# Kernel tuning notes

Measured on AMD Instinct MI355X. Metric: run time of the kernel, lower is better.

## Reference

```python
import jax, jax.numpy as jnp
import numpy as np

C = 1.5          # Poincare ball curvature (geoopt PoincareBallExact(c=1.5))
TEMP = 0.1       # logits temperature
EPS = 1e-5       # artanh clamp, matches geoopt fp32 eps


def _mlp(x, w1, b1, w2, b2, w3, b3):
    # torch nn.GELU default is the exact erf formulation
    h = jax.nn.gelu(x @ w1 + b1, approximate=False)
    h = jax.nn.gelu(h @ w2 + b2, approximate=False)
    return h @ w3 + b3


def _expmap0(u):
    # geoopt expmap0: tanh(sqrt(c)*||u||) * u / (sqrt(c)*||u||)
    sqrt_c = jnp.sqrt(C)
    n = jnp.maximum(jnp.linalg.norm(u, axis=-1, keepdims=True), 1e-15)
    return jnp.tanh(sqrt_c * n) * u / (sqrt_c * n)


def _poincare_dist(protos, y):
    """Pairwise Poincare distance. protos: (P, d) on-ball, y: (B, d) on-ball -> (B, P).
    dist(x, y) = 2/sqrt(c) * artanh(sqrt(c) * ||mobius_add(-x, y)||)
    """
    sqrt_c = jnp.sqrt(C)
    x = -protos                               # (P, d)
    x2 = jnp.sum(x * x, axis=-1)              # (P,)
    y2 = jnp.sum(y * y, axis=-1)              # (B,)
    xy = y @ x.T                              # (B, P) = <x, y> broadcast
    a = 1.0 + 2.0 * C * xy + C * y2[:, None]  # coeff of x
    b = 1.0 - C * x2[None, :]                 # coeff of y
    denom = 1.0 + 2.0 * C * xy + (C * C) * x2[None, :] * y2[:, None]
    denom = jnp.maximum(jnp.abs(denom), 1e-15)
    # only one (B, P, d) intermediate: the mobius-add numerator
    num = a[:, :, None] * x[None, :, :] + b[:, :, None] * y[:, None, :]
    r = sqrt_c * jnp.linalg.norm(num, axis=-1) / denom   # (B, P)
    r = jnp.clip(r, 0.0, 1.0 - EPS)
    return (2.0 / sqrt_c) * jnp.arctanh(r)


def setup_inputs() -> dict:
    key = jax.random.key(0)
    ks = jax.random.split(key, 16)
    B, DIN, H, D = 64, 768, 4096, 256
    PG, PS = 500, 5000

    def lin(kw, kb, fan_in, fan_out):
        s = 1.0 / np.sqrt(fan_in)
        w = jax.random.uniform(kw, (fan_in, fan_out), jnp.float32, -s, s)
        b = jax.random.uniform(kb, (fan_out,), jnp.float32, -s, s)
        return w, b

    x = jax.random.normal(ks[0], (B, DIN), jnp.float32)
    # prototypes: random points well inside the ball (radius 1/sqrt(1.5) ~ 0.816)
    protos_genus = 0.01 * jax.random.normal(ks[1], (PG, D), jnp.float32)
    protos_species = 0.01 * jax.random.normal(ks[2], (PS, D), jnp.float32)

    w1g, b1g = lin(ks[3], ks[4], DIN, H)
    w2g, b2g = lin(ks[5], ks[6], H, H)
    w3g, b3g = lin(ks[7], ks[8], H, D)
    w1s, b1s = lin(ks[9], ks[10], DIN, H)
    w2s, b2s = lin(ks[11], ks[12], H, H)
    w3s, b3s = lin(ks[13], ks[14], H, D)

    return {
        "x": x, "protos_genus": protos_genus, "protos_species": protos_species,
        "w1g": w1g, "b1g": b1g, "w2g": w2g, "b2g": b2g, "w3g": w3g, "b3g": b3g,
        "w1s": w1s, "b1s": b1s, "w2s": w2s, "b2s": b2s, "w3s": w3s, "b3s": b3s,
    }


def reference(x, protos_genus, protos_species,
              w1g, b1g, w2g, b2g, w3g, b3g,
              w1s, b1s, w2s, b2s, w3s, b3s):
    feat_g = _mlp(x, w1g, b1g, w2g, b2g, w3g, b3g)   # (B, D) euclidean
    feat_s = _mlp(x, w1s, b1s, w2s, b2s, w3s, b3s)
    hyp_g = _expmap0(feat_g)
    hyp_s = _expmap0(feat_s)
    logits_g = -_poincare_dist(protos_genus, hyp_g) / TEMP    # (B, PG)
    logits_s = -_poincare_dist(protos_species, hyp_s) / TEMP  # (B, PS)
    return (logits_g, logits_s)
```

## Files before the change

kernel.cpp:

```cpp
#include <hip/hip_runtime.h>
#include <hip/hip_bf16.h>
#include <math.h>

typedef unsigned short ushort_t;
typedef unsigned int uint_t;

#define C_CURV 1.5f
#define SQRT_C 1.22474487139158905f
#define TEMP_ 0.1f

typedef __attribute__((ext_vector_type(8))) short short8;
typedef __attribute__((ext_vector_type(4))) float f32x4;

static __device__ __forceinline__ ushort_t f2bf(float f) {
  union { float f; uint_t u; } v; v.f = f;
  uint_t u = v.u;
  uint_t r = (u + 0x7FFFu + ((u >> 16) & 1u)) >> 16;
  return (ushort_t)r;
}

static __device__ __forceinline__ float b2f(ushort_t h) {
  union { uint_t u; float f; } v; v.u = ((uint_t)h) << 16;
  return v.f;
}

static __device__ __forceinline__ float gelu_exact(float x) {
  return 0.5f * x * (1.0f + erff(x * 0.70710678118654752f));
}

__global__ void k_cvt_x(const float* __restrict__ x, ushort_t* __restrict__ xb, int n4) {
  int i = blockIdx.x * blockDim.x + threadIdx.x;
  if (i >= n4) return;
  float4 v = reinterpret_cast<const float4*>(x)[i];
  ushort4 o;
  o.x = f2bf(v.x); o.y = f2bf(v.y); o.z = f2bf(v.z); o.w = f2bf(v.w);
  reinterpret_cast<ushort4*>(xb)[i] = o;
}

__global__ __launch_bounds__(512, 4) void k_gemm(
    const ushort_t* __restrict__ Abase, long a_br_stride,
    const float* __restrict__ Wg, const float* __restrict__ Ws,
    ushort_t* __restrict__ partial, int N, int K, int kchunk)
{
  __shared__ float    sW[2][64][128];
  __shared__ ushort_t sA[2][64][64];

  const int tn = blockIdx.x, ks = blockIdx.y, br = blockIdx.z;
  const int KS = gridDim.y;
  const ushort_t* A = Abase + (long)br * a_br_stride;
  const float* W = br ? Ws : Wg;
  const int tid = threadIdx.x;
  const int lane = tid & 63;
  const int w = tid >> 6;
  const int c = lane & 15;
  const int g = lane >> 4;
  const int n0b = tn * 128;
  const int k0 = ks * kchunk;

  const int srow = tid >> 3;
  const int wcol = (tid & 7) * 16;
  const int akoff = (tid & 7) * 8;

  const float* wst = W + (long)(k0 + srow) * N + n0b + wcol;
  const ushort_t* ast = A + (long)srow * K + k0 + akoff;

  f32x4 acc[4];
  #pragma unroll
  for (int mi = 0; mi < 4; ++mi) acc[mi] = f32x4{0.f, 0.f, 0.f, 0.f};

  float4 wvA0, wvA1, wvA2, wvA3; uint4 avA;
  float4 wvB0, wvB1, wvB2, wvB3; uint4 avB;
  float4 wvC0, wvC1, wvC2, wvC3; uint4 avC;

#define LOADREG(S, T) do { \
    const float* wp_ = wst + (long)((T) * 64) * N; \
    wv##S##0 = *reinterpret_cast<const float4*>(wp_); \
    wv##S##1 = *reinterpret_cast<const float4*>(wp_ + 4); \
    wv##S##2 = *reinterpret_cast<const float4*>(wp_ + 8); \
    wv##S##3 = *reinterpret_cast<const float4*>(wp_ + 12); \
    av##S = *reinterpret_cast<const uint4*>(ast + (T) * 64); \
  } while (0)

#define DSWRITE(S, B) do { \
    float4* wd_ = reinterpret_cast<float4*>(&sW[B][srow][wcol]); \
    wd_[0] = wv##S##0; wd_[1] = wv##S##1; wd_[2] = wv##S##2; wd_[3] = wv##S##3; \
    *reinterpret_cast<uint4*>(&sA[B][srow][akoff]) = av##S; \
  } while (0)

#define COMPUTE(B) do { \
    _Pragma("unroll") for (int kk = 0; kk < 64; kk += 32) { \
      short8 af[4]; \
      _Pragma("unroll") for (int mi = 0; mi < 4; ++mi) \
        af[mi] = *reinterpret_cast<const short8*>(&sA[B][c + 16 * mi][kk + 8 * g]); \
      float bw[8]; \
      _Pragma("unroll") for (int j = 0; j < 8; ++j) \
        bw[j] = sW[B][kk + 8 * g + j][w * 16 + c]; \
      short8 bf; \
      _Pragma("unroll") for (int j = 0; j < 8; ++j) bf[j] = (short)f2bf(bw[j]); \
      _Pragma("unroll") for (int mi = 0; mi < 4; ++mi) \
        acc[mi] = __builtin_amdgcn_mfma_f32_16x16x32_bf16(af[mi], bf, acc[mi], 0, 0, 0); \
    } \
  } while (0)

#define ITER(CUR, NXT2, T) do { \
    if ((T) + 2 < nt) LOADREG(NXT2, (T) + 2); \
    __builtin_amdgcn_sched_barrier(0); \
    DSWRITE(CUR, (T) & 1); \
    asm volatile("s_waitcnt lgkmcnt(0)" ::: "memory"); \
    __builtin_amdgcn_sched_barrier(0); \
    __builtin_amdgcn_s_barrier(); \
    __builtin_amdgcn_sched_barrier(0); \
    COMPUTE((T) & 1); \
  } while (0)

  const int nt = kchunk >> 6;
  LOADREG(A, 0);
  if (nt > 1) LOADREG(B, 1);
  for (int t = 0; t < nt; t += 3) {
    ITER(A, C, t);
    if (t + 1 < nt) ITER(B, A, t + 1);
    if (t + 2 < nt) ITER(C, B, t + 2);
  }
#undef LOADREG
#undef DSWRITE
#undef COMPUTE
#undef ITER

  ushort_t* po = partial + (long)(br * KS + ks) * 64 * N;
  const int n0 = n0b + w * 16 + c;
  #pragma unroll
  for (int mi = 0; mi < 4; ++mi)
    #pragma unroll
    for (int q = 0; q < 4; ++q) {
      int b = 16 * mi + 4 * g + q;
      po[(long)b * N + n0] = f2bf(acc[mi][q]);
    }
}

__global__ void k_reduce_gelu(const ushort_t* __restrict__ partial,
    const float* __restrict__ bg, const float* __restrict__ bs,
    ushort_t* __restrict__ hb, int N, int KS, int total8)
{
  int i = blockIdx.x * blockDim.x + threadIdx.x;
  if (i >= total8) return;
  int perbr8 = 64 * N / 8;
  int br = i / perbr8;
  int rem = i - br * perbr8;
  const short8* pp = reinterpret_cast<const short8*>(partial) + (long)br * KS * perbr8 + rem;
  float s[8] = {0.f, 0.f, 0.f, 0.f, 0.f, 0.f, 0.f, 0.f};
  for (int ks = 0; ks < KS; ++ks) {
    short8 t = pp[(long)ks * perbr8];
    #pragma unroll
    for (int j = 0; j < 8; ++j) s[j] += b2f((ushort_t)t[j]);
  }
  int n8 = rem % (N / 8);
  float4 bv0 = reinterpret_cast<const float4*>(br ? bs : bg)[n8 * 2];
  float4 bv1 = reinterpret_cast<const float4*>(br ? bs : bg)[n8 * 2 + 1];
  s[0] += bv0.x; s[1] += bv0.y; s[2] += bv0.z; s[3] += bv0.w;
  s[4] += bv1.x; s[5] += bv1.y; s[6] += bv1.z; s[7] += bv1.w;
  short8 o;
  #pragma unroll
  for (int j = 0; j < 8; ++j) o[j] = (short)f2bf(gelu_exact(s[j]));
  reinterpret_cast<short8*>(hb)[i] = o;
}

__global__ __launch_bounds__(256) void k_expmap(const ushort_t* __restrict__ partial,
    const float* __restrict__ b3g, const float* __restrict__ b3s,
    ushort_t* __restrict__ hypb, float* __restrict__ y2, int KS)
{
  int b = blockIdx.x, br = blockIdx.y, d = threadIdx.x;
  const ushort_t* pp = partial + (long)(br * KS) * 64 * 256 + (long)b * 256 + d;
  float s = 0.f;
  #pragma unroll 8
  for (int ks = 0; ks < KS; ++ks) s += b2f(pp[(long)ks * 64 * 256]);
  s += (br ? b3s : b3g)[d];

  float v = s * s;
  #pragma unroll
  for (int off = 1; off < 64; off <<= 1) v += __shfl_xor(v, off);
  __shared__ float red[4];
  __shared__ float n2s;
  if ((threadIdx.x & 63) == 0) red[threadIdx.x >> 6] = v;
  __syncthreads();
  if (threadIdx.x == 0) n2s = red[0] + red[1] + red[2] + red[3];
  __syncthreads();
  float n = fmaxf(sqrtf(n2s), 1e-15f);
  float sn = SQRT_C * n;
  float t = tanhf(sn);
  float scale = t / sn;
  hypb[((long)br * 64 + b) * 256 + d] = f2bf(s * scale);
  if (threadIdx.x == 0) y2[br * 64 + b] = t * t / C_CURV;
}

__global__ __launch_bounds__(256) void k_dist(const float* __restrict__ pg,
    const float* __restrict__ ps, const ushort_t* __restrict__ hypb,
    const float* __restrict__ y2, float* __restrict__ out)
{
  int u = blockIdx.x * 4 + (threadIdx.x >> 6);
  const int lane = threadIdx.x & 63;
  const int c = lane & 15, g = lane >> 4;
  const float* protos; const ushort_t* A; const float* y2p; float* ob; int P;
  if (u < 128) {
    protos = pg; P = 500; A = hypb; y2p = y2; ob = out;
  } else {
    u -= 128;
    if (u >= 1252) return;
    protos = ps; P = 5000; A = hypb + 64 * 256; y2p = y2 + 64; ob = out + 64 * 500;
  }
  const int w = u >> 2;
  const int mi = u & 3;
  int p = w * 16 + c;
  int pc = min(p, P - 1);
  const float* pp = protos + (long)pc * 256 + 8 * g;
  const ushort_t* ap = A + (long)(c + 16 * mi) * 256 + 8 * g;

  f32x4 acc = {0.f, 0.f, 0.f, 0.f};
  float x2p = 0.f;

  #pragma unroll
  for (int s8 = 0; s8 < 8; ++s8) {
    float4 v0 = *reinterpret_cast<const float4*>(pp + 32 * s8);
    float4 v1 = *reinterpret_cast<const float4*>(pp + 32 * s8 + 4);
    x2p += v0.x * v0.x + v0.y * v0.y + v0.z * v0.z + v0.w * v0.w
         + v1.x * v1.x + v1.y * v1.y + v1.z * v1.z + v1.w * v1.w;
    short8 bfr;
    bfr[0] = (short)f2bf(v0.x); bfr[1] = (short)f2bf(v0.y);
    bfr[2] = (short)f2bf(v0.z); bfr[3] = (short)f2bf(v0.w);
    bfr[4] = (short)f2bf(v1.x); bfr[5] = (short)f2bf(v1.y);
    bfr[6] = (short)f2bf(v1.z); bfr[7] = (short)f2bf(v1.w);
    short8 af = *reinterpret_cast<const short8*>(ap + 32 * s8);
    acc = __builtin_amdgcn_mfma_f32_16x16x32_bf16(af, bfr, acc, 0, 0, 0);
  }
  x2p += __shfl_xor(x2p, 16);
  x2p += __shfl_xor(x2p, 32);
  const float x2 = x2p;
  const float bb = 1.f - C_CURV * x2;
  const float LC = -2.f / (SQRT_C * TEMP_);

  if (p < P) {
    #pragma unroll
    for (int q = 0; q < 4; ++q) {
      int b = 16 * mi + 4 * g + q;
      float xy = -acc[q];
      float y2v = y2p[b];
      float a = 1.f + 2.f * C_CURV * xy + C_CURV * y2v;
      float den = fabsf(1.f + 2.f * C_CURV * xy + C_CURV * C_CURV * x2 * y2v);
      den = fmaxf(den, 1e-15f);
      float num2 = a * a * x2 + 2.f * a * bb * xy + bb * bb * y2v;
      num2 = fmaxf(num2, 0.f);
      float r = SQRT_C * sqrtf(num2) / den;
      r = fminf(r, 1.f - 1e-5f);
      r = fmaxf(r, 0.f);
      ob[(long)b * P + p] = LC * atanhf(r);
    }
  }
}

extern "C" void kernel_launch(void* const* d_in, const int* in_sizes, int n_in,
                              void* d_out, int out_size, void* d_ws, size_t ws_size,
                              hipStream_t stream) {
  const float* x   = (const float*)d_in[0];
  const float* pg  = (const float*)d_in[1];
  const float* ps  = (const float*)d_in[2];
  const float* w1g = (const float*)d_in[3];
  const float* b1g = (const float*)d_in[4];
  const float* w2g = (const float*)d_in[5];
  const float* b2g = (const float*)d_in[6];
  const float* w3g = (const float*)d_in[7];
  const float* b3g = (const float*)d_in[8];
  const float* w1s = (const float*)d_in[9];
  const float* b1s = (const float*)d_in[10];
  const float* w2s = (const float*)d_in[11];
  const float* b2s = (const float*)d_in[12];
  const float* w3s = (const float*)d_in[13];
  const float* b3s = (const float*)d_in[14];
  float* out = (float*)d_out;
  char* ws = (char*)d_ws;
  (void)in_sizes; (void)n_in; (void)out_size; (void)ws_size;

  const int KS1 = 6, KS2 = 8, KS3 = 32;
  size_t PART = (size_t)KS2 * 2 * 64 * 4096 * 2;

  ushort_t* partial = (ushort_t*)(ws);
  ushort_t* xb      = (ushort_t*)(ws + PART);
  ushort_t* h1b     = (ushort_t*)(ws + PART + 98304);
  ushort_t* h2b     = (ushort_t*)(ws + PART + 98304 + 1048576);
  ushort_t* hypb    = (ushort_t*)(ws + PART + 98304 + 2097152);
  float*    y2      = (float*)   (ws + PART + 98304 + 2097152 + 65536);

  k_cvt_x<<<48, 256, 0, stream>>>(x, xb, 64 * 768 / 4);
  k_gemm<<<dim3(32, KS1, 2), 512, 0, stream>>>(xb, 0L, w1g, w1s, partial, 4096, 768, 768 / KS1);
  k_reduce_gelu<<<256, 256, 0, stream>>>(partial, b1g, b1s, h1b, 4096, KS1, 2 * 64 * 4096 / 8);
  k_gemm<<<dim3(32, KS2, 2), 512, 0, stream>>>(h1b, (long)64 * 4096, w2g, w2s, partial, 4096, 4096, 4096 / KS2);
  k_reduce_gelu<<<256, 256, 0, stream>>>(partial, b2g, b2s, h2b, 4096, KS2, 2 * 64 * 4096 / 8);
  k_gemm<<<dim3(2, KS3, 2), 512, 0, stream>>>(h2b, (long)64 * 4096, w3g, w3s, partial, 256, 4096, 4096 / KS3);
  k_expmap<<<dim3(64, 2), 256, 0, stream>>>(partial, b3g, b3s, hypb, y2, KS3);
  k_dist<<<345, 256, 0, stream>>>(pg, ps, hypb, y2, out);
}
```

Measured before the change: 77.67 us.

## Add triple-buffered direct global-to-LDS GEMM for layers one and three

Adds a new GEMM kernel that streams weight and activation tiles straight into LDS with global_load_lds. It uses a three-stage ring buffer over 32-wide K tiles, fencing each stage with explicit vmcnt waits and barriers. The new kernel runs for the first and third MLP layers, while the old register-staged kernel is kept for the large middle layer. Layer one's split-K factor changes from 6 to 8 so its chunk size fits the 32-wide tiling. The aim is to overlap memory loads with MFMA work and drop the register round trip, at the cost of more partial-sum traffic for layer one.

Result: no change. 76.46 us (-1.6%).

```diff
diff --git a/kernel.cpp b/kernel.cpp
--- a/kernel.cpp
+++ b/kernel.cpp
@@ -27,6 +27,10 @@
 static __device__ __forceinline__ float gelu_exact(float x) {
   return 0.5f * x * (1.0f + erff(x * 0.70710678118654752f));
 }
+
+#define GLOAD_LDS16(gp, lp) __builtin_amdgcn_global_load_lds( \
+    (const __attribute__((address_space(1))) void*)(const void*)(gp), \
+    (__attribute__((address_space(3))) void*)(void*)(lp), 16, 0, 0)
 
 __global__ void k_cvt_x(const float* __restrict__ x, ushort_t* __restrict__ xb, int n4) {
   int i = blockIdx.x * blockDim.x + threadIdx.x;
@@ -37,7 +41,81 @@
   reinterpret_cast<ushort4*>(xb)[i] = o;
 }
 
-__global__ __launch_bounds__(512, 4) void k_gemm(
+__global__ __launch_bounds__(512, 4) void k_gemm_gl(
+    const ushort_t* __restrict__ Abase, long a_br_stride,
+    const float* __restrict__ Wg, const float* __restrict__ Ws,
+    ushort_t* __restrict__ partial, int N, int K, int kchunk)
+{
+  __shared__ float    sW[3][32][128];
+  __shared__ ushort_t sA[3][64][32];
+
+  const int tn = blockIdx.x, ks = blockIdx.y, br = blockIdx.z;
+  const int KS = gridDim.y;
+  const ushort_t* A = Abase + (long)br * a_br_stride;
+  const float* W = br ? Ws : Wg;
+  const int lane = threadIdx.x & 63;
+  const int w = threadIdx.x >> 6;
+  const int c = lane & 15;
+  const int g = lane >> 4;
+  const int n0b = tn * 128;
+  const int k0 = ks * kchunk;
+  const bool hasA = (w < 4);
+
+  const float* wst = W + (long)(k0 + w * 4 + (lane >> 5)) * N + n0b + (lane & 31) * 4;
+  const ushort_t* ast = A + (long)(w * 16 + (lane >> 2)) * K + k0 + (lane & 3) * 8;
+
+  f32x4 acc[4];
+  #pragma unroll
+  for (int mi = 0; mi < 4; ++mi) acc[mi] = f32x4{0.f, 0.f, 0.f, 0.f};
+
+#define STAGE(buf, t) do { \
+    GLOAD_LDS16(wst + (long)((t) * 32) * N,     &sW[buf][w * 4][0]); \
+    GLOAD_LDS16(wst + (long)((t) * 32 + 2) * N, &sW[buf][w * 4 + 2][0]); \
+    if (hasA) GLOAD_LDS16(ast + (t) * 32, &sA[buf][w * 16][0]); \
+  } while (0)
+
+#define COMPUTE(buf) do { \
+    short8 af[4]; \
+    _Pragma("unroll") for (int mi = 0; mi < 4; ++mi) \
+      af[mi] = *reinterpret_cast<const short8*>(&sA[buf][c + 16 * mi][8 * g]); \
+    float bw[8]; \
+    _Pragma("unroll") for (int j = 0; j < 8; ++j) \
+      bw[j] = sW[buf][8 * g + j][w * 16 + c]; \
+    short8 bf; \
+    _Pragma("unroll") for (int j = 0; j < 8; ++j) bf[j] = (short)f2bf(bw[j]); \
+    _Pragma("unroll") for (int mi = 0; mi < 4; ++mi) \
+      acc[mi] = __builtin_amdgcn_mfma_f32_16x16x32_bf16(af[mi], bf, acc[mi], 0, 0, 0); \
+  } while (0)
+
+  const int nt = kchunk >> 5;
+  STAGE(0, 0);
+  STAGE(1, 1);
+  int t = 0;
+  for (; t < nt - 1; ++t) {
+    if (hasA) asm volatile("s_waitcnt vmcnt(3)" ::: "memory");
+    else      asm volatile("s_waitcnt vmcnt(2)" ::: "memory");
+    __builtin_amdgcn_s_barrier();
+    if (t + 2 < nt) STAGE((t + 2) % 3, t + 2);
+    COMPUTE(t % 3);
+  }
+  asm volatile("s_waitcnt vmcnt(0)" ::: "memory");
+  __builtin_amdgcn_s_barrier();
+  COMPUTE(t % 3);
+#undef STAGE
+#undef COMPUTE
+
+  ushort_t* po = partial + (long)(br * KS + ks) * 64 * N;
+  const int n0 = n0b + w * 16 + c;
+  #pragma unroll
+  for (int mi = 0; mi < 4; ++mi)
+    #pragma unroll
+    for (int q = 0; q < 4; ++q) {
+      int b = 16 * mi + 4 * g + q;
+      po[(long)b * N + n0] = f2bf(acc[mi][q]);
+    }
+}
+
+__global__ __launch_bounds__(512, 4) void k_gemm_rs(
     const ushort_t* __restrict__ Abase, long a_br_stride,
     const float* __restrict__ Wg, const float* __restrict__ Ws,
     ushort_t* __restrict__ partial, int N, int K, int kchunk)
@@ -278,7 +356,7 @@
   char* ws = (char*)d_ws;
   (void)in_sizes; (void)n_in; (void)out_size; (void)ws_size;
 
-  const int KS1 = 6, KS2 = 8, KS3 = 32;
+  const int KS1 = 8, KS2 = 8, KS3 = 32;
   size_t PART = (size_t)KS2 * 2 * 64 * 4096 * 2;
 
   ushort_t* partial = (ushort_t*)(ws);
@@ -289,11 +367,11 @@
   float*    y2      = (float*)   (ws + PART + 98304 + 2097152 + 65536);
 
   k_cvt_x<<<48, 256, 0, stream>>>(x, xb, 64 * 768 / 4);
-  k_gemm<<<dim3(32, KS1, 2), 512, 0, stream>>>(xb, 0L, w1g, w1s, partial, 4096, 768, 768 / KS1);
+  k_gemm_gl<<<dim3(32, KS1, 2), 512, 0, stream>>>(xb, 0L, w1g, w1s, partial, 4096, 768, 768 / KS1);
   k_reduce_gelu<<<256, 256, 0, stream>>>(partial, b1g, b1s, h1b, 4096, KS1, 2 * 64 * 4096 / 8);
-  k_gemm<<<dim3(32, KS2, 2), 512, 0, stream>>>(h1b, (long)64 * 4096, w2g, w2s, partial, 4096, 4096, 4096 / KS2);
+  k_gemm_rs<<<dim3(32, KS2, 2), 512, 0, stream>>>(h1b, (long)64 * 4096, w2g, w2s, partial, 4096, 4096, 4096 / KS2);
   k_reduce_gelu<<<256, 256, 0, stream>>>(partial, b2g, b2s, h2b, 4096, KS2, 2 * 64 * 4096 / 8);
-  k_gemm<<<dim3(2, KS3, 2), 512, 0, stream>>>(h2b, (long)64 * 4096, w3g, w3s, partial, 256, 4096, 4096 / KS3);
+  k_gemm_gl<<<dim3(2, KS3, 2), 512, 0, stream>>>(h2b, (long)64 * 4096, w3g, w3s, partial, 256, 4096, 4096 / KS3);
   k_expmap<<<dim3(64, 2), 256, 0, stream>>>(partial, b3g, b3s, hypb, y2, KS3);
   k_dist<<<345, 256, 0, stream>>>(pg, ps, hypb, y2, out);
 }
```
